# Performance work log

Measured on AMD Instinct MI355X. Metric: run time of the kernel, lower is better.

Reference implementation:

```python
import jax, jax.numpy as jnp
import numpy as np

B, T, QD, AD = 64, 4096, 1024, 256
SCORE_MASK_VALUE = -1e30


def setup_inputs() -> dict:
    key = jax.random.key(0)
    k1, k2, k3, k4, k5 = jax.random.split(key, 5)
    query = jax.random.normal(k1, (B, QD), dtype=jnp.float32)
    processed_memory = jax.random.normal(k2, (B, T, AD), dtype=jnp.float32)
    mask = jax.random.randint(k3, (B, T), 0, 2).astype(bool)
    Wq = jax.random.normal(k4, (AD, QD), dtype=jnp.float32) * (1.0 / np.sqrt(QD))
    v = jax.random.normal(k5, (AD,), dtype=jnp.float32) * (1.0 / np.sqrt(AD))
    return {"query": query, "processed_memory": processed_memory, "mask": mask, "Wq": Wq, "v": v}


def reference(query, processed_memory, mask, Wq, v):
    # processed_query: (B, AD) -> broadcast over time
    processed_query = query @ Wq.T                      # (B, AD)
    hidden = jnp.tanh(processed_query[:, None, :] + processed_memory)  # (B, T, AD)
    energies = jnp.einsum('btd,d->bt', hidden, v)       # (B, T)
    energies = jnp.where(mask, SCORE_MASK_VALUE, energies)
    alignment = jax.nn.softmax(energies, axis=1)        # (B, T)
    return alignment
```

## Files before the change

### kernel.cpp

```cpp
#include <hip/hip_runtime.h>
#include <math.h>

#define B_  64
#define T_  4096
#define QD_ 1024
#define AD_ 256
#define MASKVAL (-1e30f)
#define LOG2E 1.44269504f
#define RS_STRIDE 32

__device__ __forceinline__ float tanh_fast(float x) {
    float xc = fminf(fmaxf(x, -9.0f), 9.0f);
    float e  = __builtin_amdgcn_exp2f(xc * (2.0f * LOG2E));
    return (e - 1.0f) * __builtin_amdgcn_rcpf(e + 1.0f);
}

__global__ __launch_bounds__(256) void pq_kernel(const float* __restrict__ query,
                                                 const float* __restrict__ Wq,
                                                 float* __restrict__ pq) {
    const int wave = threadIdx.x >> 6;
    const int lane = threadIdx.x & 63;
    const int w = blockIdx.x * 4 + wave;
    const int b = w >> 8;
    const int d = w & 255;

    const float4* q4 = (const float4*)(query + (size_t)b * QD_);
    const float4* w4 = (const float4*)(Wq + (size_t)d * QD_);
    float sum = 0.f;
#pragma unroll
    for (int j = 0; j < QD_ / 4 / 64; ++j) {
        const float4 a = q4[j * 64 + lane];
        const float4 c = w4[j * 64 + lane];
        sum += a.x * c.x + a.y * c.y + a.z * c.z + a.w * c.w;
    }
#pragma unroll
    for (int off = 32; off > 0; off >>= 1)
        sum += __shfl_xor(sum, off, 64);
    if (lane == 0) pq[w] = sum;
}

__global__ __launch_bounds__(256) void energy_kernel(const float* __restrict__ pm,
                                                     const int*   __restrict__ mask,
                                                     const float* __restrict__ pq,
                                                     const float* __restrict__ v,
                                                     float* __restrict__ expv,
                                                     float* __restrict__ rowsum) {
    const int wave = threadIdx.x >> 6;
    const int lane = threadIdx.x & 63;
    const size_t grp = (size_t)blockIdx.x * 4 + wave;
    const size_t t0  = grp * 4;
    const int b = (int)(t0 >> 12);
    __shared__ float wsum[4];

    const int4 mk = ((const int4*)mask)[grp];
    const int msk0 = __builtin_amdgcn_readfirstlane(mk.x);
    const int msk1 = __builtin_amdgcn_readfirstlane(mk.y);
    const int msk2 = __builtin_amdgcn_readfirstlane(mk.z);
    const int msk3 = __builtin_amdgcn_readfirstlane(mk.w);
    const int msk[4] = {msk0, msk1, msk2, msk3};

    const float4 q  = ((const float4*)(pq + (size_t)b * AD_))[lane];
    const float4 vv = ((const float4*)v)[lane];

    const float4* pm4 = (const float4*)pm;
    float4 m[4];
#pragma unroll
    for (int i = 0; i < 4; ++i)
        if (!msk[i]) m[i] = pm4[(t0 + i) * (AD_ / 4) + lane];

    float res[4];
#pragma unroll
    for (int i = 0; i < 4; ++i) {
        if (msk[i]) { res[i] = 0.0f; continue; }
        float e = tanh_fast(q.x + m[i].x) * vv.x
                + tanh_fast(q.y + m[i].y) * vv.y
                + tanh_fast(q.z + m[i].z) * vv.z
                + tanh_fast(q.w + m[i].w) * vv.w;
#pragma unroll
        for (int off = 32; off > 0; off >>= 1)
            e += __shfl_xor(e, off, 64);
        res[i] = __builtin_amdgcn_exp2f(e * LOG2E);
    }
    if (lane == 0) {
        ((float4*)expv)[grp] = make_float4(res[0], res[1], res[2], res[3]);
        wsum[wave] = res[0] + res[1] + res[2] + res[3];
    }
    __syncthreads();
    if (threadIdx.x == 0)
        atomicAdd(&rowsum[b * RS_STRIDE], wsum[0] + wsum[1] + wsum[2] + wsum[3]);
}

__global__ __launch_bounds__(256) void scale_kernel(const float* __restrict__ expv,
                                                    const float* __restrict__ rowsum,
                                                    float* __restrict__ out) {
    const size_t i = (size_t)blockIdx.x * 256 + threadIdx.x;
    const int b = (int)(i >> 10);
    const float inv = 1.0f / rowsum[b * RS_STRIDE];
    float4 e = ((const float4*)expv)[i];
    e.x *= inv; e.y *= inv; e.z *= inv; e.w *= inv;
    ((float4*)out)[i] = e;
}

extern "C" void kernel_launch(void* const* d_in, const int* in_sizes, int n_in,
                              void* d_out, int out_size, void* d_ws, size_t ws_size,
                              hipStream_t stream) {
    const float* query = (const float*)d_in[0];
    const float* pm    = (const float*)d_in[1];
    const int*   mask  = (const int*)  d_in[2];
    const float* Wq    = (const float*)d_in[3];
    const float* v     = (const float*)d_in[4];
    float* out = (float*)d_out;

    float* pq     = (float*)d_ws;
    float* expv   = pq + (size_t)B_ * AD_;
    float* rowsum = expv + (size_t)B_ * T_;

    hipMemsetAsync(rowsum, 0, B_ * RS_STRIDE * sizeof(float), stream);
    pq_kernel<<<(B_ * AD_) / 4, 256, 0, stream>>>(query, Wq, pq);
    energy_kernel<<<(B_ * T_) / 16, 256, 0, stream>>>(pm, mask, pq, v, expv, rowsum);
    scale_kernel<<<(B_ * T_) / 1024, 256, 0, stream>>>(expv, rowsum, out);
}
```

Baseline: 343.9 us.

## Split wave into quarter-wave timesteps, use tanh identity, fold rowsum zeroing into pq

Each wave now handles four timesteps, with 16 lanes per timestep, so the cross-lane reduction is a 16-lane butterfly instead of four full 64-lane reductions. The tanh is rewritten as v·tanh(x) = v − 2v/(exp(2x)+1), which drops the clamp and a subtract per element. The hipMemsetAsync of the row sums is replaced by zeroing inside block 0 of pq_kernel, removing one launch. Risks: each lane's memory access pattern changes (float4 loads strided by sub*4), and dropping the clamp relies on exp2 overflowing cleanly to inf.

After: 347.2 us. Within noise of the previous version (+1.0%).

```diff
diff --git a/kernel.cpp b/kernel.cpp
--- a/kernel.cpp
+++ b/kernel.cpp
@@ -5,19 +5,18 @@
 #define T_  4096
 #define QD_ 1024
 #define AD_ 256
-#define MASKVAL (-1e30f)
 #define LOG2E 1.44269504f
 #define RS_STRIDE 32
 
-__device__ __forceinline__ float tanh_fast(float x) {
-    float xc = fminf(fmaxf(x, -9.0f), 9.0f);
-    float e  = __builtin_amdgcn_exp2f(xc * (2.0f * LOG2E));
-    return (e - 1.0f) * __builtin_amdgcn_rcpf(e + 1.0f);
-}
-
 __global__ __launch_bounds__(256) void pq_kernel(const float* __restrict__ query,
                                                  const float* __restrict__ Wq,
-                                                 float* __restrict__ pq) {
+                                                 float* __restrict__ pq,
+                                                 float* __restrict__ rowsum) {
+    if (blockIdx.x == 0) {
+        const float4 z = make_float4(0.f, 0.f, 0.f, 0.f);
+        ((float4*)rowsum)[threadIdx.x]       = z;
+        ((float4*)rowsum)[threadIdx.x + 256] = z;
+    }
     const int wave = threadIdx.x >> 6;
     const int lane = threadIdx.x & 63;
     const int w = blockIdx.x * 4 + wave;
@@ -47,44 +46,46 @@
                                                      float* __restrict__ rowsum) {
     const int wave = threadIdx.x >> 6;
     const int lane = threadIdx.x & 63;
-    const size_t grp = (size_t)blockIdx.x * 4 + wave;
-    const size_t t0  = grp * 4;
+    const int qt   = lane >> 4;
+    const int sub  = lane & 15;
+    const size_t t0 = ((size_t)blockIdx.x * 4 + wave) * 4;
+    const size_t t  = t0 + qt;
     const int b = (int)(t0 >> 12);
     __shared__ float wsum[4];
 
-    const int4 mk = ((const int4*)mask)[grp];
-    const int msk0 = __builtin_amdgcn_readfirstlane(mk.x);
-    const int msk1 = __builtin_amdgcn_readfirstlane(mk.y);
-    const int msk2 = __builtin_amdgcn_readfirstlane(mk.z);
-    const int msk3 = __builtin_amdgcn_readfirstlane(mk.w);
-    const int msk[4] = {msk0, msk1, msk2, msk3};
+    const int mk = mask[t];
 
-    const float4 q  = ((const float4*)(pq + (size_t)b * AD_))[lane];
-    const float4 vv = ((const float4*)v)[lane];
+    const float4* q4 = (const float4*)(pq + (size_t)b * AD_) + sub * 4;
+    const float4* v4 = ((const float4*)v) + sub * 4;
+    const float4* m4 = (const float4*)(pm + t * AD_) + sub * 4;
 
-    const float4* pm4 = (const float4*)pm;
-    float4 m[4];
+    const float C = 2.0f * LOG2E;
+    float acc = 0.f, vsum = 0.f;
 #pragma unroll
-    for (int i = 0; i < 4; ++i)
-        if (!msk[i]) m[i] = pm4[(t0 + i) * (AD_ / 4) + lane];
+    for (int j = 0; j < 4; ++j) {
+        const float4 vv = v4[j];
+        const float4 qq = q4[j];
+        float4 mm = make_float4(0.f, 0.f, 0.f, 0.f);
+        if (!mk) mm = m4[j];
+        vsum += vv.x + vv.y + vv.z + vv.w;
+        const float r0 = __builtin_amdgcn_rcpf(__builtin_amdgcn_exp2f((qq.x + mm.x) * C) + 1.0f);
+        const float r1 = __builtin_amdgcn_rcpf(__builtin_amdgcn_exp2f((qq.y + mm.y) * C) + 1.0f);
+        const float r2 = __builtin_amdgcn_rcpf(__builtin_amdgcn_exp2f((qq.z + mm.z) * C) + 1.0f);
+        const float r3 = __builtin_amdgcn_rcpf(__builtin_amdgcn_exp2f((qq.w + mm.w) * C) + 1.0f);
+        acc += vv.x * r0 + vv.y * r1 + vv.z * r2 + vv.w * r3;
+    }
+    float e = vsum - 2.0f * acc;
+#pragma unroll
+    for (int off = 1; off < 16; off <<= 1)
+        e += __shfl_xor(e, off, 64);
 
-    float res[4];
-#pragma unroll
-    for (int i = 0; i < 4; ++i) {
-        if (msk[i]) { res[i] = 0.0f; continue; }
-        float e = tanh_fast(q.x + m[i].x) * vv.x
-                + tanh_fast(q.y + m[i].y) * vv.y
-                + tanh_fast(q.z + m[i].z) * vv.z
-                + tanh_fast(q.w + m[i].w) * vv.w;
-#pragma unroll
-        for (int off = 32; off > 0; off >>= 1)
-            e += __shfl_xor(e, off, 64);
-        res[i] = __builtin_amdgcn_exp2f(e * LOG2E);
-    }
-    if (lane == 0) {
-        ((float4*)expv)[grp] = make_float4(res[0], res[1], res[2], res[3]);
-        wsum[wave] = res[0] + res[1] + res[2] + res[3];
-    }
+    const float res = mk ? 0.0f : __builtin_amdgcn_exp2f(e * LOG2E);
+    if (sub == 0) expv[t] = res;
+
+    float ws = res;
+    ws += __shfl_xor(ws, 16, 64);
+    ws += __shfl_xor(ws, 32, 64);
+    if (lane == 0) wsum[wave] = ws;
     __syncthreads();
     if (threadIdx.x == 0)
         atomicAdd(&rowsum[b * RS_STRIDE], wsum[0] + wsum[1] + wsum[2] + wsum[3]);
@@ -115,8 +116,7 @@
     float* expv   = pq + (size_t)B_ * AD_;
     float* rowsum = expv + (size_t)B_ * T_;
 
-    hipMemsetAsync(rowsum, 0, B_ * RS_STRIDE * sizeof(float), stream);
-    pq_kernel<<<(B_ * AD_) / 4, 256, 0, stream>>>(query, Wq, pq);
+    pq_kernel<<<(B_ * AD_) / 4, 256, 0, stream>>>(query, Wq, pq, rowsum);
     energy_kernel<<<(B_ * T_) / 16, 256, 0, stream>>>(pm, mask, pq, v, expv, rowsum);
     scale_kernel<<<(B_ * T_) / 1024, 256, 0, stream>>>(expv, rowsum, out);
 }
```
